# Optimization experiments

Measured on AMD Instinct MI355X. Metric: run time of the kernel, lower is better.

Reference implementation:

```python
import jax, jax.numpy as jnp
import numpy as np

SHAPE = (32, 512, 512)  # (D, H, W) dense voxel grid
N_ACTIVE = 150000


def setup_inputs() -> dict:
    key = jax.random.key(0)
    k_f, k_w1, k_w2 = jax.random.split(key, 3)
    D, H, W = SHAPE
    # unique active voxel coordinates (collision-free dense-grid hash)
    rng = np.random.default_rng(0)
    lin = rng.permutation(D * H * W)[:N_ACTIVE]
    z = lin // (H * W)
    y = (lin // W) % H
    x = lin % W
    coors = np.stack([np.zeros(N_ACTIVE, np.int32), z.astype(np.int32),
                      y.astype(np.int32), x.astype(np.int32)], axis=1)
    features = jax.random.normal(k_f, (N_ACTIVE, 3), dtype=jnp.float32)
    # per-offset GEMM weights: [K^3, Cin, Cout]
    w1 = jax.random.normal(k_w1, (27, 3, 128), dtype=jnp.float32) * 0.2
    w2 = jax.random.normal(k_w2, (27, 128, 128), dtype=jnp.float32) * 0.05
    return {"features": features, "coors": jnp.asarray(coors), "w1": w1,
            "w2": w2, "batch_size": 1}


def _build_grid(coors):
    D, H, W = SHAPE
    n = coors.shape[0]
    grid = jnp.full((D, H, W), -1, dtype=jnp.int32)
    return grid.at[coors[:, 1], coors[:, 2], coors[:, 3]].set(
        jnp.arange(n, dtype=jnp.int32))


def _subm_conv3d(feat, coors, grid, w):
    """Submanifold 3x3x3 conv: gather active neighbors per offset, GEMM, accumulate.
    feat: [N, Cin]; w: [27, Cin, Cout]; output defined only on active sites -> [N, Cout]."""
    D, H, W = SHAPE
    n = feat.shape[0]
    out = jnp.zeros((n, w.shape[-1]), dtype=feat.dtype)
    k = 0
    for dz in (-1, 0, 1):
        for dy in (-1, 0, 1):
            for dx in (-1, 0, 1):
                nz = coors[:, 1] + dz
                ny = coors[:, 2] + dy
                nx = coors[:, 3] + dx
                inb = ((nz >= 0) & (nz < D) & (ny >= 0) & (ny < H)
                       & (nx >= 0) & (nx < W))
                nidx = grid[jnp.clip(nz, 0, D - 1), jnp.clip(ny, 0, H - 1),
                            jnp.clip(nx, 0, W - 1)]
                valid = inb & (nidx >= 0)
                g = jnp.where(valid[:, None],
                              feat[jnp.clip(nidx, 0, n - 1)], 0.0)  # [N, Cin]
                out = out + g @ w[k]
                k += 1
    return out


def reference(features, coors, w1, w2, batch_size):
    # SparseConvTensor: features [N,3], coors [N,4] (batch,z,y,x), batch_size=1
    grid = _build_grid(coors)
    h = _subm_conv3d(features, coors, grid, w1)   # SubMConv3d(3, 128, 3)
    out = _subm_conv3d(h, coors, grid, w2)        # SubMConv3d(128, 128, 3), shared indice_key
    return out
```

## Files before the change

### kernel.cpp

```cpp
#include <hip/hip_runtime.h>
#include <stdint.h>

#define GD 32
#define GH 512
#define GW 512
#define GDHW (GD * GH * GW)
#define KOFF 27
#define CAP 4096
#define CNTS 32

typedef __attribute__((ext_vector_type(8))) short short8;
typedef __attribute__((ext_vector_type(4))) float f32x4;

typedef const __attribute__((address_space(1))) unsigned int* gu32p;
typedef __attribute__((address_space(3))) unsigned int* lu32p;

__device__ __forceinline__ void async_load16(const void* g, void* l) {
    __builtin_amdgcn_global_load_lds((gu32p)g, (lu32p)l, 16, 0, 0);
}

__device__ __forceinline__ unsigned short f32_to_bf16(float x) {
    unsigned int u = __float_as_uint(x);
    unsigned int r = (u + 0x7FFFu + ((u >> 16) & 1u)) >> 16;
    return (unsigned short)r;
}

__global__ void scatter_kernel(const int* __restrict__ coors,
                               int* __restrict__ grid, int n) {
    int i = blockIdx.x * 256 + threadIdx.x;
    if (i >= n) return;
    int z = coors[i * 4 + 1];
    int y = coors[i * 4 + 2];
    int x = coors[i * 4 + 3];
    grid[(z * GH + y) * GW + x] = i;
}

__global__ __launch_bounds__(256) void nbr_kernel(
    const int* __restrict__ coors, const int* __restrict__ grid,
    int* __restrict__ vcnt, int* __restrict__ nbrc,
    int2* __restrict__ pairs, int* __restrict__ cnts, int n) {
    __shared__ int wcnt[4][26];
    __shared__ int kbase[26];

    const int i = blockIdx.x * 256 + threadIdx.x;
    const int t = threadIdx.x, wave = t >> 6, lane = t & 63;
    const bool live = (i < n);
    const unsigned long long lmask = (1ull << lane) - 1;

    int z = 0, y = 0, x = 0;
    if (live) {
        z = coors[i * 4 + 1];
        y = coors[i * 4 + 2];
        x = coors[i * 4 + 3];
    }

    int j[27];
#pragma unroll
    for (int k = 0; k < 27; ++k) {
        if (k == 13) { j[k] = live ? i : -1; continue; }
        int dz = k / 9 - 1, dy = (k / 3) % 3 - 1, dx = k % 3 - 1;
        int nz = z + dz, ny = y + dy, nx = x + dx;
        int cz = min(max(nz, 0), GD - 1);
        int cy = min(max(ny, 0), GH - 1);
        int cx = min(max(nx, 0), GW - 1);
        int jj = grid[(cz * GH + cy) * GW + cx];
        bool ok = live && nz >= 0 && nz < GD && ny >= 0 && ny < GH &&
                  nx >= 0 && nx < GW;
        j[k] = ok ? jj : -1;
    }

    if (live) {
        int c = 0;
#pragma unroll
        for (int k = 0; k < 27; ++k) {
            if (k == 13) continue;
            if (j[k] >= 0) { nbrc[i * 27 + c] = (k << 20) | j[k]; ++c; }
        }
        vcnt[i] = c;
    }

#pragma unroll
    for (int kk = 0; kk < 26; ++kk) {
        const int k = kk + (kk >= 13);
        unsigned long long m = __ballot(live && (j[k] >= 0));
        if (lane == 0) wcnt[wave][kk] = __popcll(m);
    }
    __syncthreads();
    if (t < 26) {
        int tot = wcnt[0][t] + wcnt[1][t] + wcnt[2][t] + wcnt[3][t];
        kbase[t] = (tot > 0) ? atomicAdd(&cnts[t * CNTS], tot) : 0;
    }
    __syncthreads();
#pragma unroll
    for (int kk = 0; kk < 26; ++kk) {
        const int k = kk + (kk >= 13);
        const bool valid = live && (j[k] >= 0);
        unsigned long long m = __ballot(valid);
        if (valid) {
            int off = 0;
#pragma unroll
            for (int w = 0; w < 4; ++w)
                if (w < wave) off += wcnt[w][kk];
            int pos = kbase[kk] + off + __popcll(m & lmask);
            if (pos < CAP) pairs[kk * CAP + pos] = make_int2(i, j[k]);
        }
    }
}

__global__ void w2prep_kernel(const float* __restrict__ w2,
                              unsigned short* __restrict__ w2s) {
    int g = blockIdx.x * 256 + threadIdx.x;
    if (g >= KOFF * 128 * 128) return;
    int k = g >> 14;
    int c = (g >> 7) & 127;
    int idx = g & 127;
    int cc = idx >> 3, e = idx & 7;
    int scc = ((cc & 7) ^ (c & 7)) | (cc & 8);
    int cin = scc * 8 + e;
    w2s[g] = f32_to_bf16(w2[(k * 128 + cin) * 128 + c]);
}

__global__ __launch_bounds__(256) void conv1_kernel(
    const float* __restrict__ feat, const float* __restrict__ w1,
    const int* __restrict__ vcnt, const int* __restrict__ nbrc,
    unsigned short* __restrict__ hout, int n) {
    const int wave = threadIdx.x >> 6, lane = threadIdx.x & 63;
    const int i = blockIdx.x * 4 + wave;
    if (i >= n) return;
    const int c2 = lane * 2;

    const int cnt = vcnt[i];
    float f0 = feat[i * 3 + 0];
    float f1 = feat[i * 3 + 1];
    float f2 = feat[i * 3 + 2];

    const float* wc = w1 + 13 * 384 + c2;
    float2 w0 = *(const float2*)(wc);
    float2 wv1 = *(const float2*)(wc + 128);
    float2 w2_ = *(const float2*)(wc + 256);
    float a0 = f0 * w0.x + f1 * wv1.x + f2 * w2_.x;
    float a1 = f0 * w0.y + f1 * wv1.y + f2 * w2_.y;

    for (int s = 0; s < cnt; ++s) {
        int e = nbrc[i * 27 + s];
        int k = e >> 20, j = e & 0xFFFFF;
        float g0 = feat[j * 3 + 0];
        float g1 = feat[j * 3 + 1];
        float g2 = feat[j * 3 + 2];
        const float* wk = w1 + k * 384 + c2;
        float2 u0 = *(const float2*)(wk);
        float2 u1 = *(const float2*)(wk + 128);
        float2 u2 = *(const float2*)(wk + 256);
        a0 += g0 * u0.x + g1 * u1.x + g2 * u2.x;
        a1 += g0 * u0.y + g1 * u1.y + g2 * u2.y;
    }

    unsigned int packed = (unsigned int)f32_to_bf16(a0) |
                          ((unsigned int)f32_to_bf16(a1) << 16);
    *(unsigned int*)(hout + (size_t)i * 128 + c2) = packed;
}

__global__ __launch_bounds__(256, 2) void conv2a_kernel(
    const unsigned short* __restrict__ h,
    const unsigned short* __restrict__ w2s,
    const unsigned short* __restrict__ zeropage,
    float* __restrict__ out, int n) {
    __shared__ __align__(16) unsigned char Alds[32768];
    __shared__ __align__(16) unsigned char Blds[32768];

    const int t = threadIdx.x;
    const int wave = t >> 6, lane = t & 63;
    const int lane16 = lane & 15, quad = lane >> 4;
    const int wm = wave >> 1, wn = wave & 1;
    const int row0 = blockIdx.x * 128;

    if (wave < 2) {
        const int rbase = wave * 64;
#pragma unroll
        for (int it = 0; it < 16; ++it) {
            int r = rbase + it * 4 + quad;
            int i = row0 + r;
            int scc = ((lane & 7) ^ (r & 7)) | (lane & 8);
            const unsigned short* src =
                (i < n) ? (h + (size_t)i * 128 + scc * 8) : (zeropage + scc * 8);
            async_load16(src, &Alds[(rbase + it * 4) * 256]);
        }
    } else {
        const int rbase = (wave - 2) * 64;
        const unsigned short* w2k = w2s + 13 * 16384;
#pragma unroll
        for (int it = 0; it < 16; ++it) {
            int chunk = (rbase + it * 4) * 16 + lane;
            async_load16(w2k + chunk * 8, &Blds[(rbase + it * 4) * 256]);
        }
    }

    f32x4 acc[4][4];
#pragma unroll
    for (int a = 0; a < 4; ++a)
#pragma unroll
        for (int b = 0; b < 4; ++b) acc[a][b] = (f32x4){0.f, 0.f, 0.f, 0.f};

    __syncthreads();

#pragma unroll
    for (int ks = 0; ks < 4; ++ks) {
        const int q = ks * 4 + quad;
        short8 a[4];
#pragma unroll
        for (int ms = 0; ms < 4; ++ms) {
            int m = wm * 64 + ms * 16 + lane16;
            int pos = ((q & 7) ^ (m & 7)) | (q & 8);
            a[ms] = *(const short8*)&Alds[m * 256 + pos * 16];
        }
#pragma unroll
        for (int ns = 0; ns < 4; ++ns) {
            int c = wn * 64 + ns * 16 + lane16;
            int pos = ((q & 7) ^ (c & 7)) | (q & 8);
            short8 b = *(const short8*)&Blds[c * 256 + pos * 16];
#pragma unroll
            for (int ms = 0; ms < 4; ++ms)
                acc[ms][ns] = __builtin_amdgcn_mfma_f32_16x16x32_bf16(
                    a[ms], b, acc[ms][ns], 0, 0, 0);
        }
    }

#pragma unroll
    for (int ms = 0; ms < 4; ++ms) {
#pragma unroll
        for (int r = 0; r < 4; ++r) {
            int i = row0 + wm * 64 + ms * 16 + quad * 4 + r;
            if (i < n) {
#pragma unroll
                for (int ns = 0; ns < 4; ++ns) {
                    int col = wn * 64 + ns * 16 + lane16;
                    out[(size_t)i * 128 + col] = acc[ms][ns][r];
                }
            }
        }
    }
}

__global__ __launch_bounds__(256, 2) void conv2b_kernel(
    const unsigned short* __restrict__ h,
    const unsigned short* __restrict__ w2s,
    const int2* __restrict__ pairs, const int* __restrict__ cnts,
    const unsigned short* __restrict__ zeropage,
    float* __restrict__ out, int n) {
    __shared__ __align__(16) unsigned char Alds[32768];
    __shared__ __align__(16) unsigned char Blds[32768];

    const int kb = blockIdx.x >> 5;
    const int tile = blockIdx.x & 31;
    const int cnt = min(cnts[kb * CNTS], CAP);
    const int base = tile * 128;
    if (base >= cnt) return;
    const int m = min(128, cnt - base);
    const int k = kb + (kb >= 13);
    const int2* pk = pairs + kb * CAP + base;

    const int t = threadIdx.x;
    const int wave = t >> 6, lane = t & 63;
    const int lane16 = lane & 15, quad = lane >> 4;
    const int wm = wave >> 1, wn = wave & 1;

    if (wave < 2) {
        const int rbase = wave * 64;
#pragma unroll
        for (int it = 0; it < 16; ++it) {
            int r = rbase + it * 4 + quad;
            int j = (r < m) ? pk[r].y : -1;
            int scc = ((lane & 7) ^ (r & 7)) | (lane & 8);
            const unsigned short* src =
                (j >= 0) ? (h + (size_t)j * 128 + scc * 8) : (zeropage + scc * 8);
            async_load16(src, &Alds[(rbase + it * 4) * 256]);
        }
    } else {
        const int rbase = (wave - 2) * 64;
        const unsigned short* w2k = w2s + k * 16384;
#pragma unroll
        for (int it = 0; it < 16; ++it) {
            int chunk = (rbase + it * 4) * 16 + lane;
            async_load16(w2k + chunk * 8, &Blds[(rbase + it * 4) * 256]);
        }
    }

    f32x4 acc[4][4];
#pragma unroll
    for (int a = 0; a < 4; ++a)
#pragma unroll
        for (int b = 0; b < 4; ++b) acc[a][b] = (f32x4){0.f, 0.f, 0.f, 0.f};

    __syncthreads();

#pragma unroll
    for (int ks = 0; ks < 4; ++ks) {
        const int q = ks * 4 + quad;
        short8 a[4];
#pragma unroll
        for (int ms = 0; ms < 4; ++ms) {
            int mm = wm * 64 + ms * 16 + lane16;
            int pos = ((q & 7) ^ (mm & 7)) | (q & 8);
            a[ms] = *(const short8*)&Alds[mm * 256 + pos * 16];
        }
#pragma unroll
        for (int ns = 0; ns < 4; ++ns) {
            int c = wn * 64 + ns * 16 + lane16;
            int pos = ((q & 7) ^ (c & 7)) | (q & 8);
            short8 b = *(const short8*)&Blds[c * 256 + pos * 16];
#pragma unroll
            for (int ms = 0; ms < 4; ++ms)
                acc[ms][ns] = __builtin_amdgcn_mfma_f32_16x16x32_bf16(
                    a[ms], b, acc[ms][ns], 0, 0, 0);
        }
    }

#pragma unroll
    for (int ms = 0; ms < 4; ++ms) {
#pragma unroll
        for (int r = 0; r < 4; ++r) {
            int row = wm * 64 + ms * 16 + quad * 4 + r;
            if (row < m) {
                int pi = pk[row].x;
#pragma unroll
                for (int ns = 0; ns < 4; ++ns) {
                    int col = wn * 64 + ns * 16 + lane16;
                    unsafeAtomicAdd(&out[(size_t)pi * 128 + col], acc[ms][ns][r]);
                }
            }
        }
    }
}

extern "C" void kernel_launch(void* const* d_in, const int* in_sizes, int n_in,
                              void* d_out, int out_size, void* d_ws,
                              size_t ws_size, hipStream_t stream) {
    const float* feat = (const float*)d_in[0];
    const int* coors = (const int*)d_in[1];
    const float* w1 = (const float*)d_in[2];
    const float* w2 = (const float*)d_in[3];
    float* out = (float*)d_out;

    const int n = in_sizes[0] / 3;

    uint8_t* ws = (uint8_t*)d_ws;
    size_t off = 0;
    int* grid = (int*)(ws + off); off += (size_t)GDHW * 4;
    int* vcnt = (int*)(ws + off); off += (size_t)n * 4;
    int* nbrc = (int*)(ws + off); off += (size_t)n * 27 * 4;
    off = (off + 255) & ~(size_t)255;
    unsigned short* hbuf = (unsigned short*)(ws + off);
    off += (size_t)n * 128 * 2;
    off = (off + 255) & ~(size_t)255;
    unsigned short* w2s = (unsigned short*)(ws + off);
    off += (size_t)KOFF * 128 * 128 * 2;
    off = (off + 255) & ~(size_t)255;
    int2* pairs = (int2*)(ws + off);
    off += (size_t)26 * CAP * sizeof(int2);
    off = (off + 255) & ~(size_t)255;
    int* cnts = (int*)(ws + off); off += 26 * CNTS * 4;
    off = (off + 255) & ~(size_t)255;
    unsigned short* zerop = (unsigned short*)(ws + off); off += 256;

    hipMemsetAsync(grid, 0xFF, (size_t)GDHW * 4, stream);
    hipMemsetAsync(vcnt, 0x00, (size_t)n * 4, stream);
    hipMemsetAsync(cnts, 0x00, 26 * CNTS * 4, stream);
    hipMemsetAsync(zerop, 0x00, 256, stream);

    int nb = (n + 255) / 256;
    scatter_kernel<<<nb, 256, 0, stream>>>(coors, grid, n);
    w2prep_kernel<<<(KOFF * 128 * 128 + 255) / 256, 256, 0, stream>>>(w2, w2s);
    nbr_kernel<<<nb, 256, 0, stream>>>(coors, grid, vcnt, nbrc, pairs, cnts, n);
    conv1_kernel<<<(n + 3) / 4, 256, 0, stream>>>(feat, w1, vcnt, nbrc, hbuf, n);
    conv2a_kernel<<<(n + 127) / 128, 256, 0, stream>>>(hbuf, w2s, zerop, out, n);
    conv2b_kernel<<<26 * 32, 256, 0, stream>>>(hbuf, w2s, pairs, cnts, zerop,
                                               out, n);
}
```

Measured before the change: 239.9 us.

## Replace atomic scatter of neighbor GEMM results with gathered epilogue in center conv

```diff
diff --git a/kernel.cpp b/kernel.cpp
--- a/kernel.cpp
+++ b/kernel.cpp
@@ -8,6 +8,7 @@
 #define KOFF 27
 #define CAP 4096
 #define CNTS 32
+#define NW2 (KOFF * 128 * 128)
 
 typedef __attribute__((ext_vector_type(8))) short short8;
 typedef __attribute__((ext_vector_type(4))) float f32x4;
@@ -25,20 +26,43 @@
     return (unsigned short)r;
 }
 
-__global__ void scatter_kernel(const int* __restrict__ coors,
-                               int* __restrict__ grid, int n) {
-    int i = blockIdx.x * 256 + threadIdx.x;
-    if (i >= n) return;
-    int z = coors[i * 4 + 1];
-    int y = coors[i * 4 + 2];
-    int x = coors[i * 4 + 3];
-    grid[(z * GH + y) * GW + x] = i;
+__global__ __launch_bounds__(256) void setup_kernel(
+    const int* __restrict__ coors, int* __restrict__ grid,
+    const float* __restrict__ w2, unsigned short* __restrict__ w2s,
+    int* __restrict__ cnts, unsigned short* __restrict__ zerop,
+    int n, int nbsc) {
+    const int bid = blockIdx.x, t = threadIdx.x;
+    if (bid == 0) {
+        for (int q = t; q < 26 * CNTS; q += 256) cnts[q] = 0;
+        if (t < 64) ((int*)zerop)[t] = 0;
+    }
+    if (bid < nbsc) {
+        int i = bid * 256 + t;
+        if (i < n) {
+            int z = coors[i * 4 + 1];
+            int y = coors[i * 4 + 2];
+            int x = coors[i * 4 + 3];
+            grid[(z * GH + y) * GW + x] = i;
+        }
+    } else {
+        int g = (bid - nbsc) * 256 + t;
+        if (g < NW2) {
+            int k = g >> 14;
+            int c = (g >> 7) & 127;
+            int idx = g & 127;
+            int cc = idx >> 3, e = idx & 7;
+            int scc = ((cc & 7) ^ (c & 7)) | (cc & 8);
+            int cin = scc * 8 + e;
+            w2s[g] = f32_to_bf16(w2[(k * 128 + cin) * 128 + c]);
+        }
+    }
 }
 
 __global__ __launch_bounds__(256) void nbr_kernel(
     const int* __restrict__ coors, const int* __restrict__ grid,
     int* __restrict__ vcnt, int* __restrict__ nbrc,
-    int2* __restrict__ pairs, int* __restrict__ cnts, int n) {
+    int* __restrict__ pairs, int* __restrict__ npos,
+    int* __restrict__ cnts, int n) {
     __shared__ int wcnt[4][26];
     __shared__ int kbase[26];
 
@@ -91,6 +115,7 @@
         kbase[t] = (tot > 0) ? atomicAdd(&cnts[t * CNTS], tot) : 0;
     }
     __syncthreads();
+    int slot = 0;
 #pragma unroll
     for (int kk = 0; kk < 26; ++kk) {
         const int k = kk + (kk >= 13);
@@ -102,22 +127,15 @@
             for (int w = 0; w < 4; ++w)
                 if (w < wave) off += wcnt[w][kk];
             int pos = kbase[kk] + off + __popcll(m & lmask);
-            if (pos < CAP) pairs[kk * CAP + pos] = make_int2(i, j[k]);
-        }
-    }
-}
-
-__global__ void w2prep_kernel(const float* __restrict__ w2,
-                              unsigned short* __restrict__ w2s) {
-    int g = blockIdx.x * 256 + threadIdx.x;
-    if (g >= KOFF * 128 * 128) return;
-    int k = g >> 14;
-    int c = (g >> 7) & 127;
-    int idx = g & 127;
-    int cc = idx >> 3, e = idx & 7;
-    int scc = ((cc & 7) ^ (c & 7)) | (cc & 8);
-    int cin = scc * 8 + e;
-    w2s[g] = f32_to_bf16(w2[(k * 128 + cin) * 128 + c]);
+            if (pos < CAP) {
+                pairs[kk * CAP + pos] = j[k];
+                npos[i * 27 + slot] = kk * CAP + pos;
+            } else {
+                npos[i * 27 + slot] = -1;
+            }
+            ++slot;
+        }
+    }
 }
 
 __global__ __launch_bounds__(256) void conv1_kernel(
@@ -160,10 +178,103 @@
     *(unsigned int*)(hout + (size_t)i * 128 + c2) = packed;
 }
 
+__global__ __launch_bounds__(256, 2) void conv2b_kernel(
+    const unsigned short* __restrict__ h,
+    const unsigned short* __restrict__ w2s,
+    const int* __restrict__ pairs, const int* __restrict__ cnts,
+    const unsigned short* __restrict__ zeropage,
+    float* __restrict__ corr) {
+    __shared__ __align__(16) unsigned char Alds[32768];
+    __shared__ __align__(16) unsigned char Blds[32768];
+
+    const int kb = blockIdx.x >> 5;
+    const int tile = blockIdx.x & 31;
+    const int cnt = min(cnts[kb * CNTS], CAP);
+    const int base = tile * 128;
+    if (base >= cnt) return;
+    const int m = min(128, cnt - base);
+    const int k = kb + (kb >= 13);
+    const int* pk = pairs + kb * CAP + base;
+
+    const int t = threadIdx.x;
+    const int wave = t >> 6, lane = t & 63;
+    const int lane16 = lane & 15, quad = lane >> 4;
+    const int wm = wave >> 1, wn = wave & 1;
+
+    if (wave < 2) {
+        const int rbase = wave * 64;
+#pragma unroll
+        for (int it = 0; it < 16; ++it) {
+            int r = rbase + it * 4 + quad;
+            int j = (r < m) ? pk[r] : -1;
+            int scc = ((lane & 7) ^ (r & 7)) | (lane & 8);
+            const unsigned short* src =
+                (j >= 0) ? (h + (size_t)j * 128 + scc * 8) : (zeropage + scc * 8);
+            async_load16(src, &Alds[(rbase + it * 4) * 256]);
+        }
+    } else {
+        const int rbase = (wave - 2) * 64;
+        const unsigned short* w2k = w2s + k * 16384;
+#pragma unroll
+        for (int it = 0; it < 16; ++it) {
+            int chunk = (rbase + it * 4) * 16 + lane;
+            async_load16(w2k + chunk * 8, &Blds[(rbase + it * 4) * 256]);
+        }
+    }
+
+    f32x4 acc[4][4];
+#pragma unroll
+    for (int a = 0; a < 4; ++a)
+#pragma unroll
+        for (int b = 0; b < 4; ++b) acc[a][b] = (f32x4){0.f, 0.f, 0.f, 0.f};
+
+    __syncthreads();
+
+#pragma unroll
+    for (int ks = 0; ks < 4; ++ks) {
+        const int q = ks * 4 + quad;
+        short8 a[4];
+#pragma unroll
+        for (int ms = 0; ms < 4; ++ms) {
+            int mm = wm * 64 + ms * 16 + lane16;
+            int pos = ((q & 7) ^ (mm & 7)) | (q & 8);
+            a[ms] = *(const short8*)&Alds[mm * 256 + pos * 16];
+        }
+#pragma unroll
+        for (int ns = 0; ns < 4; ++ns) {
+            int c = wn * 64 + ns * 16 + lane16;
+            int pos = ((q & 7) ^ (c & 7)) | (q & 8);
+            short8 b = *(const short8*)&Blds[c * 256 + pos * 16];
+#pragma unroll
+            for (int ms = 0; ms < 4; ++ms)
+                acc[ms][ns] = __builtin_amdgcn_mfma_f32_16x16x32_bf16(
+                    a[ms], b, acc[ms][ns], 0, 0, 0);
+        }
+    }
+
+#pragma unroll
+    for (int ms = 0; ms < 4; ++ms) {
+#pragma unroll
+        for (int r = 0; r < 4; ++r) {
+            int row = wm * 64 + ms * 16 + quad * 4 + r;
+            if (row < m) {
+                float* cr = corr + (size_t)(kb * CAP + base + row) * 128;
+#pragma unroll
+                for (int ns = 0; ns < 4; ++ns) {
+                    int col = wn * 64 + ns * 16 + lane16;
+                    cr[col] = acc[ms][ns][r];
+                }
+            }
+        }
+    }
+}
+
 __global__ __launch_bounds__(256, 2) void conv2a_kernel(
     const unsigned short* __restrict__ h,
     const unsigned short* __restrict__ w2s,
     const unsigned short* __restrict__ zeropage,
+    const int* __restrict__ vcnt, const int* __restrict__ npos,
+    const float* __restrict__ corr,
     float* __restrict__ out, int n) {
     __shared__ __align__(16) unsigned char Alds[32768];
     __shared__ __align__(16) unsigned char Blds[32768];
@@ -231,101 +342,23 @@
         for (int r = 0; r < 4; ++r) {
             int i = row0 + wm * 64 + ms * 16 + quad * 4 + r;
             if (i < n) {
+                const int cnt = vcnt[i];
+                const int* np = npos + i * 27;
+                for (int s = 0; s < cnt; ++s) {
+                    int p = np[s];
+                    if (p >= 0) {
+                        const float* cr =
+                            corr + (size_t)p * 128 + wn * 64 + lane16;
+                        acc[ms][0][r] += cr[0];
+                        acc[ms][1][r] += cr[16];
+                        acc[ms][2][r] += cr[32];
+                        acc[ms][3][r] += cr[48];
+                    }
+                }
 #pragma unroll
                 for (int ns = 0; ns < 4; ++ns) {
                     int col = wn * 64 + ns * 16 + lane16;
                     out[(size_t)i * 128 + col] = acc[ms][ns][r];
-                }
-            }
-        }
-    }
-}
-
-__global__ __launch_bounds__(256, 2) void conv2b_kernel(
-    const unsigned short* __restrict__ h,
-    const unsigned short* __restrict__ w2s,
-    const int2* __restrict__ pairs, const int* __restrict__ cnts,
-    const unsigned short* __restrict__ zeropage,
-    float* __restrict__ out, int n) {
-    __shared__ __align__(16) unsigned char Alds[32768];
-    __shared__ __align__(16) unsigned char Blds[32768];
-
-    const int kb = blockIdx.x >> 5;
-    const int tile = blockIdx.x & 31;
-    const int cnt = min(cnts[kb * CNTS], CAP);
-    const int base = tile * 128;
-    if (base >= cnt) return;
-    const int m = min(128, cnt - base);
-    const int k = kb + (kb >= 13);
-    const int2* pk = pairs + kb * CAP + base;
-
-    const int t = threadIdx.x;
-    const int wave = t >> 6, lane = t & 63;
-    const int lane16 = lane & 15, quad = lane >> 4;
-    const int wm = wave >> 1, wn = wave & 1;
-
-    if (wave < 2) {
-        const int rbase = wave * 64;
-#pragma unroll
-        for (int it = 0; it < 16; ++it) {
-            int r = rbase + it * 4 + quad;
-            int j = (r < m) ? pk[r].y : -1;
-            int scc = ((lane & 7) ^ (r & 7)) | (lane & 8);
-            const unsigned short* src =
-                (j >= 0) ? (h + (size_t)j * 128 + scc * 8) : (zeropage + scc * 8);
-            async_load16(src, &Alds[(rbase + it * 4) * 256]);
-        }
-    } else {
-        const int rbase = (wave - 2) * 64;
-        const unsigned short* w2k = w2s + k * 16384;
-#pragma unroll
-        for (int it = 0; it < 16; ++it) {
-            int chunk = (rbase + it * 4) * 16 + lane;
-            async_load16(w2k + chunk * 8, &Blds[(rbase + it * 4) * 256]);
-        }
-    }
-
-    f32x4 acc[4][4];
-#pragma unroll
-    for (int a = 0; a < 4; ++a)
-#pragma unroll
-        for (int b = 0; b < 4; ++b) acc[a][b] = (f32x4){0.f, 0.f, 0.f, 0.f};
-
-    __syncthreads();
-
-#pragma unroll
-    for (int ks = 0; ks < 4; ++ks) {
-        const int q = ks * 4 + quad;
-        short8 a[4];
-#pragma unroll
-        for (int ms = 0; ms < 4; ++ms) {
-            int mm = wm * 64 + ms * 16 + lane16;
-            int pos = ((q & 7) ^ (mm & 7)) | (q & 8);
-            a[ms] = *(const short8*)&Alds[mm * 256 + pos * 16];
-        }
-#pragma unroll
-        for (int ns = 0; ns < 4; ++ns) {
-            int c = wn * 64 + ns * 16 + lane16;
-            int pos = ((q & 7) ^ (c & 7)) | (q & 8);
-            short8 b = *(const short8*)&Blds[c * 256 + pos * 16];
-#pragma unroll
-            for (int ms = 0; ms < 4; ++ms)
-                acc[ms][ns] = __builtin_amdgcn_mfma_f32_16x16x32_bf16(
-                    a[ms], b, acc[ms][ns], 0, 0, 0);
-        }
-    }
-
-#pragma unroll
-    for (int ms = 0; ms < 4; ++ms) {
-#pragma unroll
-        for (int r = 0; r < 4; ++r) {
-            int row = wm * 64 + ms * 16 + quad * 4 + r;
-            if (row < m) {
-                int pi = pk[row].x;
-#pragma unroll
-                for (int ns = 0; ns < 4; ++ns) {
-                    int col = wn * 64 + ns * 16 + lane16;
-                    unsafeAtomicAdd(&out[(size_t)pi * 128 + col], acc[ms][ns][r]);
                 }
             }
         }
@@ -348,6 +381,7 @@
     int* grid = (int*)(ws + off); off += (size_t)GDHW * 4;
     int* vcnt = (int*)(ws + off); off += (size_t)n * 4;
     int* nbrc = (int*)(ws + off); off += (size_t)n * 27 * 4;
+    int* npos = (int*)(ws + off); off += (size_t)n * 27 * 4;
     off = (off + 255) & ~(size_t)255;
     unsigned short* hbuf = (unsigned short*)(ws + off);
     off += (size_t)n * 128 * 2;
@@ -355,24 +389,27 @@
     unsigned short* w2s = (unsigned short*)(ws + off);
     off += (size_t)KOFF * 128 * 128 * 2;
     off = (off + 255) & ~(size_t)255;
-    int2* pairs = (int2*)(ws + off);
-    off += (size_t)26 * CAP * sizeof(int2);
+    int* pairs = (int*)(ws + off);
+    off += (size_t)26 * CAP * 4;
     off = (off + 255) & ~(size_t)255;
     int* cnts = (int*)(ws + off); off += 26 * CNTS * 4;
     off = (off + 255) & ~(size_t)255;
     unsigned short* zerop = (unsigned short*)(ws + off); off += 256;
+    off = (off + 255) & ~(size_t)255;
+    float* corr = (float*)(ws + off);
+    off += (size_t)26 * CAP * 128 * 4;
 
     hipMemsetAsync(grid, 0xFF, (size_t)GDHW * 4, stream);
-    hipMemsetAsync(vcnt, 0x00, (size_t)n * 4, stream);
-    hipMemsetAsync(cnts, 0x00, 26 * CNTS * 4, stream);
-    hipMemsetAsync(zerop, 0x00, 256, stream);
-
-    int nb = (n + 255) / 256;
-    scatter_kernel<<<nb, 256, 0, stream>>>(coors, grid, n);
-    w2prep_kernel<<<(KOFF * 128 * 128 + 255) / 256, 256, 0, stream>>>(w2, w2s);
-    nbr_kernel<<<nb, 256, 0, stream>>>(coors, grid, vcnt, nbrc, pairs, cnts, n);
+
+    const int nbsc = (n + 255) / 256;
+    const int nbw2 = (NW2 + 255) / 256;
+    setup_kernel<<<nbsc + nbw2, 256, 0, stream>>>(coors, grid, w2, w2s, cnts,
+                                                  zerop, n, nbsc);
+    nbr_kernel<<<nbsc, 256, 0, stream>>>(coors, grid, vcnt, nbrc, pairs, npos,
+                                         cnts, n);
     conv1_kernel<<<(n + 3) / 4, 256, 0, stream>>>(feat, w1, vcnt, nbrc, hbuf, n);
-    conv2a_kernel<<<(n + 127) / 128, 256, 0, stream>>>(hbuf, w2s, zerop, out, n);
     conv2b_kernel<<<26 * 32, 256, 0, stream>>>(hbuf, w2s, pairs, cnts, zerop,
-                                               out, n);
-}
+                                               corr);
+    conv2a_kernel<<<(n + 127) / 128, 256, 0, stream>>>(hbuf, w2s, zerop, vcnt,
+                                                       npos, corr, out, n);
+}
```

After: 263.6 us. +9.9%, slower.

## Load conv2 MFMA operands directly to registers and fuse setup kernels

Applied to the files above, without the earlier changes.

```diff
diff --git a/kernel.cpp b/kernel.cpp
--- a/kernel.cpp
+++ b/kernel.cpp
@@ -8,16 +8,10 @@
 #define KOFF 27
 #define CAP 4096
 #define CNTS 32
+#define NW2 (KOFF * 128 * 128)
 
 typedef __attribute__((ext_vector_type(8))) short short8;
 typedef __attribute__((ext_vector_type(4))) float f32x4;
-
-typedef const __attribute__((address_space(1))) unsigned int* gu32p;
-typedef __attribute__((address_space(3))) unsigned int* lu32p;
-
-__device__ __forceinline__ void async_load16(const void* g, void* l) {
-    __builtin_amdgcn_global_load_lds((gu32p)g, (lu32p)l, 16, 0, 0);
-}
 
 __device__ __forceinline__ unsigned short f32_to_bf16(float x) {
     unsigned int u = __float_as_uint(x);
@@ -25,14 +19,31 @@
     return (unsigned short)r;
 }
 
-__global__ void scatter_kernel(const int* __restrict__ coors,
-                               int* __restrict__ grid, int n) {
-    int i = blockIdx.x * 256 + threadIdx.x;
-    if (i >= n) return;
-    int z = coors[i * 4 + 1];
-    int y = coors[i * 4 + 2];
-    int x = coors[i * 4 + 3];
-    grid[(z * GH + y) * GW + x] = i;
+__global__ __launch_bounds__(256) void setup_kernel(
+    const int* __restrict__ coors, int* __restrict__ grid,
+    const float* __restrict__ w2, unsigned short* __restrict__ w2t,
+    int* __restrict__ cnts, int n, int nbsc) {
+    const int bid = blockIdx.x, t = threadIdx.x;
+    if (bid == 0) {
+        for (int q = t; q < 26 * CNTS; q += 256) cnts[q] = 0;
+    }
+    if (bid < nbsc) {
+        int i = bid * 256 + t;
+        if (i < n) {
+            int z = coors[i * 4 + 1];
+            int y = coors[i * 4 + 2];
+            int x = coors[i * 4 + 3];
+            grid[(z * GH + y) * GW + x] = i;
+        }
+    } else {
+        int g = (bid - nbsc) * 256 + t;
+        if (g < NW2) {
+            int k = g >> 14;
+            int c = (g >> 7) & 127;
+            int q = g & 127;
+            w2t[g] = f32_to_bf16(w2[(k * 128 + q) * 128 + c]);
+        }
+    }
 }
 
 __global__ __launch_bounds__(256) void nbr_kernel(
@@ -105,19 +116,6 @@
             if (pos < CAP) pairs[kk * CAP + pos] = make_int2(i, j[k]);
         }
     }
-}
-
-__global__ void w2prep_kernel(const float* __restrict__ w2,
-                              unsigned short* __restrict__ w2s) {
-    int g = blockIdx.x * 256 + threadIdx.x;
-    if (g >= KOFF * 128 * 128) return;
-    int k = g >> 14;
-    int c = (g >> 7) & 127;
-    int idx = g & 127;
-    int cc = idx >> 3, e = idx & 7;
-    int scc = ((cc & 7) ^ (c & 7)) | (cc & 8);
-    int cin = scc * 8 + e;
-    w2s[g] = f32_to_bf16(w2[(k * 128 + cin) * 128 + c]);
 }
 
 __global__ __launch_bounds__(256) void conv1_kernel(
@@ -162,68 +160,50 @@
 
 __global__ __launch_bounds__(256, 2) void conv2a_kernel(
     const unsigned short* __restrict__ h,
-    const unsigned short* __restrict__ w2s,
-    const unsigned short* __restrict__ zeropage,
+    const unsigned short* __restrict__ w2t,
     float* __restrict__ out, int n) {
-    __shared__ __align__(16) unsigned char Alds[32768];
-    __shared__ __align__(16) unsigned char Blds[32768];
-
     const int t = threadIdx.x;
     const int wave = t >> 6, lane = t & 63;
     const int lane16 = lane & 15, quad = lane >> 4;
     const int wm = wave >> 1, wn = wave & 1;
     const int row0 = blockIdx.x * 128;
 
-    if (wave < 2) {
-        const int rbase = wave * 64;
-#pragma unroll
-        for (int it = 0; it < 16; ++it) {
-            int r = rbase + it * 4 + quad;
-            int i = row0 + r;
-            int scc = ((lane & 7) ^ (r & 7)) | (lane & 8);
-            const unsigned short* src =
-                (i < n) ? (h + (size_t)i * 128 + scc * 8) : (zeropage + scc * 8);
-            async_load16(src, &Alds[(rbase + it * 4) * 256]);
-        }
-    } else {
-        const int rbase = (wave - 2) * 64;
-        const unsigned short* w2k = w2s + 13 * 16384;
-#pragma unroll
-        for (int it = 0; it < 16; ++it) {
-            int chunk = (rbase + it * 4) * 16 + lane;
-            async_load16(w2k + chunk * 8, &Blds[(rbase + it * 4) * 256]);
-        }
+    short8 a[4][4];
+#pragma unroll
+    for (int ms = 0; ms < 4; ++ms) {
+        int r = row0 + wm * 64 + ms * 16 + lane16;
+        r = min(r, n - 1);
+        const unsigned short* hp = h + (size_t)r * 128 + quad * 8;
+#pragma unroll
+        for (int ks = 0; ks < 4; ++ks)
+            a[ms][ks] = *(const short8*)(hp + ks * 32);
+    }
+
+    short8 b[4][4];
+    const unsigned short* wbase = w2t + 13 * 16384 + quad * 8;
+#pragma unroll
+    for (int ns = 0; ns < 4; ++ns) {
+        int c = wn * 64 + ns * 16 + lane16;
+        const unsigned short* wp = wbase + c * 128;
+#pragma unroll
+        for (int ks = 0; ks < 4; ++ks)
+            b[ns][ks] = *(const short8*)(wp + ks * 32);
     }
 
     f32x4 acc[4][4];
 #pragma unroll
-    for (int a = 0; a < 4; ++a)
-#pragma unroll
-        for (int b = 0; b < 4; ++b) acc[a][b] = (f32x4){0.f, 0.f, 0.f, 0.f};
-
-    __syncthreads();
-
-#pragma unroll
-    for (int ks = 0; ks < 4; ++ks) {
-        const int q = ks * 4 + quad;
-        short8 a[4];
-#pragma unroll
-        for (int ms = 0; ms < 4; ++ms) {
-            int m = wm * 64 + ms * 16 + lane16;
-            int pos = ((q & 7) ^ (m & 7)) | (q & 8);
-            a[ms] = *(const short8*)&Alds[m * 256 + pos * 16];
-        }
-#pragma unroll
-        for (int ns = 0; ns < 4; ++ns) {
-            int c = wn * 64 + ns * 16 + lane16;
-            int pos = ((q & 7) ^ (c & 7)) | (q & 8);
-            short8 b = *(const short8*)&Blds[c * 256 + pos * 16];
+    for (int p = 0; p < 4; ++p)
+#pragma unroll
+        for (int q = 0; q < 4; ++q) acc[p][q] = (f32x4){0.f, 0.f, 0.f, 0.f};
+
+#pragma unroll
+    for (int ks = 0; ks < 4; ++ks)
+#pragma unroll
+        for (int ns = 0; ns < 4; ++ns)
 #pragma unroll
             for (int ms = 0; ms < 4; ++ms)
                 acc[ms][ns] = __builtin_amdgcn_mfma_f32_16x16x32_bf16(
-                    a[ms], b, acc[ms][ns], 0, 0, 0);
-        }
-    }
+                    a[ms][ks], b[ns][ks], acc[ms][ns], 0, 0, 0);
 
 #pragma unroll
     for (int ms = 0; ms < 4; ++ms) {
@@ -243,13 +223,9 @@
 
 __global__ __launch_bounds__(256, 2) void conv2b_kernel(
     const unsigned short* __restrict__ h,
-    const unsigned short* __restrict__ w2s,
+    const unsigned short* __restrict__ w2t,
     const int2* __restrict__ pairs, const int* __restrict__ cnts,
-    const unsigned short* __restrict__ zeropage,
-    float* __restrict__ out, int n) {
-    __shared__ __align__(16) unsigned char Alds[32768];
-    __shared__ __align__(16) unsigned char Blds[32768];
-
+    float* __restrict__ out) {
     const int kb = blockIdx.x >> 5;
     const int tile = blockIdx.x & 31;
     const int cnt = min(cnts[kb * CNTS], CAP);
@@ -264,56 +240,44 @@
     const int lane16 = lane & 15, quad = lane >> 4;
     const int wm = wave >> 1, wn = wave & 1;
 
-    if (wave < 2) {
-        const int rbase = wave * 64;
-#pragma unroll
-        for (int it = 0; it < 16; ++it) {
-            int r = rbase + it * 4 + quad;
-            int j = (r < m) ? pk[r].y : -1;
-            int scc = ((lane & 7) ^ (r & 7)) | (lane & 8);
-            const unsigned short* src =
-                (j >= 0) ? (h + (size_t)j * 128 + scc * 8) : (zeropage + scc * 8);
-            async_load16(src, &Alds[(rbase + it * 4) * 256]);
-        }
-    } else {
-        const int rbase = (wave - 2) * 64;
-        const unsigned short* w2k = w2s + k * 16384;
-#pragma unroll
-        for (int it = 0; it < 16; ++it) {
-            int chunk = (rbase + it * 4) * 16 + lane;
-            async_load16(w2k + chunk * 8, &Blds[(rbase + it * 4) * 256]);
-        }
+    short8 a[4][4];
+#pragma unroll
+    for (int ms = 0; ms < 4; ++ms) {
+        int r = wm * 64 + ms * 16 + lane16;
+        bool v = (r < m);
+        int j = v ? pk[r].y : 0;
+        const unsigned short* hp = h + (size_t)j * 128 + quad * 8;
+#pragma unroll
+        for (int ks = 0; ks < 4; ++ks)
+            a[ms][ks] = v ? *(const short8*)(hp + ks * 32)
+                          : (short8){0, 0, 0, 0, 0, 0, 0, 0};
+    }
+
+    short8 b[4][4];
+    const unsigned short* wbase = w2t + (size_t)k * 16384 + quad * 8;
+#pragma unroll
+    for (int ns = 0; ns < 4; ++ns) {
+        int c = wn * 64 + ns * 16 + lane16;
+        const unsigned short* wp = wbase + c * 128;
+#pragma unroll
+        for (int ks = 0; ks < 4; ++ks)
+            b[ns][ks] = *(const short8*)(wp + ks * 32);
     }
 
     f32x4 acc[4][4];
 #pragma unroll
-    for (int a = 0; a < 4; ++a)
-#pragma unroll
-        for (int b = 0; b < 4; ++b) acc[a][b] = (f32x4){0.f, 0.f, 0.f, 0.f};
-
-    __syncthreads();
-
-#pragma unroll
-    for (int ks = 0; ks < 4; ++ks) {
-        const int q = ks * 4 + quad;
-        short8 a[4];
-#pragma unroll
-        for (int ms = 0; ms < 4; ++ms) {
-            int mm = wm * 64 + ms * 16 + lane16;
-            int pos = ((q & 7) ^ (mm & 7)) | (q & 8);
-            a[ms] = *(const short8*)&Alds[mm * 256 + pos * 16];
-        }
-#pragma unroll
-        for (int ns = 0; ns < 4; ++ns) {
-            int c = wn * 64 + ns * 16 + lane16;
-            int pos = ((q & 7) ^ (c & 7)) | (q & 8);
-            short8 b = *(const short8*)&Blds[c * 256 + pos * 16];
+    for (int p = 0; p < 4; ++p)
+#pragma unroll
+        for (int q = 0; q < 4; ++q) acc[p][q] = (f32x4){0.f, 0.f, 0.f, 0.f};
+
+#pragma unroll
+    for (int ks = 0; ks < 4; ++ks)
+#pragma unroll
+        for (int ns = 0; ns < 4; ++ns)
 #pragma unroll
             for (int ms = 0; ms < 4; ++ms)
                 acc[ms][ns] = __builtin_amdgcn_mfma_f32_16x16x32_bf16(
-                    a[ms], b, acc[ms][ns], 0, 0, 0);
-        }
-    }
+                    a[ms][ks], b[ns][ks], acc[ms][ns], 0, 0, 0);
 
 #pragma unroll
     for (int ms = 0; ms < 4; ++ms) {
@@ -352,27 +316,23 @@
     unsigned short* hbuf = (unsigned short*)(ws + off);
     off += (size_t)n * 128 * 2;
     off = (off + 255) & ~(size_t)255;
-    unsigned short* w2s = (unsigned short*)(ws + off);
+    unsigned short* w2t = (unsigned short*)(ws + off);
     off += (size_t)KOFF * 128 * 128 * 2;
     off = (off + 255) & ~(size_t)255;
     int2* pairs = (int2*)(ws + off);
     off += (size_t)26 * CAP * sizeof(int2);
     off = (off + 255) & ~(size_t)255;
     int* cnts = (int*)(ws + off); off += 26 * CNTS * 4;
-    off = (off + 255) & ~(size_t)255;
-    unsigned short* zerop = (unsigned short*)(ws + off); off += 256;
 
     hipMemsetAsync(grid, 0xFF, (size_t)GDHW * 4, stream);
-    hipMemsetAsync(vcnt, 0x00, (size_t)n * 4, stream);
-    hipMemsetAsync(cnts, 0x00, 26 * CNTS * 4, stream);
-    hipMemsetAsync(zerop, 0x00, 256, stream);
-
-    int nb = (n + 255) / 256;
-    scatter_kernel<<<nb, 256, 0, stream>>>(coors, grid, n);
-    w2prep_kernel<<<(KOFF * 128 * 128 + 255) / 256, 256, 0, stream>>>(w2, w2s);
-    nbr_kernel<<<nb, 256, 0, stream>>>(coors, grid, vcnt, nbrc, pairs, cnts, n);
+
+    const int nbsc = (n + 255) / 256;
+    const int nbw2 = (NW2 + 255) / 256;
+    setup_kernel<<<nbsc + nbw2, 256, 0, stream>>>(coors, grid, w2, w2t, cnts,
+                                                  n, nbsc);
+    nbr_kernel<<<nbsc, 256, 0, stream>>>(coors, grid, vcnt, nbrc, pairs, cnts,
+                                         n);
     conv1_kernel<<<(n + 3) / 4, 256, 0, stream>>>(feat, w1, vcnt, nbrc, hbuf, n);
-    conv2a_kernel<<<(n + 127) / 128, 256, 0, stream>>>(hbuf, w2s, zerop, out, n);
-    conv2b_kernel<<<26 * 32, 256, 0, stream>>>(hbuf, w2s, pairs, cnts, zerop,
-                                               out, n);
-}
+    conv2a_kernel<<<(n + 127) / 128, 256, 0, stream>>>(hbuf, w2t, out, n);
+    conv2b_kernel<<<26 * 32, 256, 0, stream>>>(hbuf, w2t, pairs, cnts, out);
+}
```

New measurement: 241.1 us. About the same (+0.5%).
